# Kernel tuning notes

Measured on AMD Instinct MI355X. Metric: run time of the kernel, lower is better.

The kernel has to match this reference:

```python
import jax, jax.numpy as jnp
import numpy as np

TEMP = 0.2
LAM = 0.5
EPS = 1e-8

N, IN_SIZE, HID = 8192, 256, 128


def setup_inputs() -> dict:
    key = jax.random.key(0)
    k1, k2, k3, k4, k5 = jax.random.split(key, 5)
    z_mp = jax.random.normal(k1, (N, IN_SIZE), dtype=jnp.float32)
    z_sc = jax.random.normal(k2, (N, IN_SIZE), dtype=jnp.float32)
    # xavier-normal-ish init scale
    W1 = jax.random.normal(k3, (IN_SIZE, HID), dtype=jnp.float32) * (1.414 * (2.0 / (IN_SIZE + HID)) ** 0.5)
    b1 = jnp.zeros((HID,), dtype=jnp.float32)
    W2 = jax.random.normal(k4, (HID, HID), dtype=jnp.float32) * (1.414 * (2.0 / (HID + HID)) ** 0.5)
    b2 = jnp.zeros((HID,), dtype=jnp.float32)
    pos = jax.random.randint(k5, (N, N), 0, 2, dtype=jnp.int32)
    return {"z_mp": z_mp, "z_sc": z_sc, "W1": W1, "b1": b1, "W2": W2, "b2": b2, "pos": pos}


def _proj(z, W1, b1, W2, b2):
    # Linear -> ELU -> Linear
    return jax.nn.elu(z @ W1 + b1) @ W2 + b2


def _l2norm(z):
    # F.normalize(p=2, dim=1): torch uses clamp_min(eps) on the norm
    n = jnp.linalg.norm(z, axis=1, keepdims=True)
    return z / jnp.maximum(n, 1e-12)


def reference(z_mp, z_sc, W1, b1, W2, b2, pos):
    zp_sc = _proj(z_sc, W1, b1, W2, b2)
    zp_mp = _proj(z_mp, W1, b1, W2, b2)
    # exp(cosine similarity / temperature), dense N x N
    sim = jnp.exp(_l2norm(zp_mp) @ _l2norm(zp_sc).T / TEMP)  # [N, N] mp2sc
    mp2sc = sim / (jnp.sum(sim, axis=1, keepdims=True) + EPS)
    sc2mp = sim.T / (jnp.sum(sim, axis=0)[:, None] + EPS)
    posf = pos.astype(sim.dtype)
    lori_sc = -jnp.log(jnp.sum(sc2mp * posf, axis=-1) + EPS)
    lori_mp = -jnp.log(jnp.sum(mp2sc * posf, axis=-1) + EPS)
    ans = LAM * lori_mp + (1.0 - LAM) * lori_sc
    ans = jnp.where(jnp.isnan(ans) | jnp.isinf(ans), jnp.zeros((), ans.dtype), ans)
    return ans
```

## Files before the change

### kernel.cpp

```cpp
#include <hip/hip_runtime.h>
#include <math.h>

#define N_ROWS 8192
#define IN_SZ 256
#define HID 128
#define INV_TEMP 5.0f
#define EPSV 1e-8f

typedef short short8 __attribute__((ext_vector_type(8)));
typedef float f32x4 __attribute__((ext_vector_type(4)));

__device__ __forceinline__ ushort f2bf(float v) {
    unsigned b = __float_as_uint(v);
    return (ushort)((b + 0x7FFFu + ((b >> 16) & 1u)) >> 16);
}
__device__ __forceinline__ float bf2f(ushort u) {
    return __uint_as_float(((unsigned)u) << 16);
}

__device__ __forceinline__ void gl2lds16(const void* g, void* l) {
    __builtin_amdgcn_global_load_lds(
        (const __attribute__((address_space(1))) unsigned*)g,
        (__attribute__((address_space(3))) unsigned*)l, 16, 0, 0);
}

__global__ __launch_bounds__(256) void pack_kernel(
    const int* __restrict__ pos, unsigned* __restrict__ posbits,
    float* __restrict__ sums)
{
    const int t = threadIdx.x;
    if (blockIdx.x < 4) {
        float4 z4 = make_float4(0.f, 0.f, 0.f, 0.f);
        float* base = sums + (size_t)blockIdx.x * 8192 + t * 32;
#pragma unroll
        for (int i = 0; i < 8; ++i) *(float4*)(base + i * 4) = z4;
    }
    const size_t nthreads = (size_t)gridDim.x * 256;
    const size_t total_groups = (size_t)N_ROWS * N_ROWS / 4;
#pragma unroll 8
    for (size_t g = (size_t)blockIdx.x * 256 + t; g < total_groups; g += nthreads) {
        int4 v = *(const int4*)(pos + g * 4);
        unsigned nib = (v.x != 0 ? 1u : 0u) | (v.y != 0 ? 2u : 0u)
                     | (v.z != 0 ? 4u : 0u) | (v.w != 0 ? 8u : 0u);
        unsigned u = nib << ((t & 7) * 4);
        u |= (unsigned)__shfl_xor((int)u, 1);
        u |= (unsigned)__shfl_xor((int)u, 2);
        u |= (unsigned)__shfl_xor((int)u, 4);
        if ((t & 7) == 0) posbits[g >> 3] = u;
    }
}

__global__ __launch_bounds__(256) void proj_kernel(
    const float* __restrict__ z_mp, const float* __restrict__ z_sc,
    const float* __restrict__ W1, const float* __restrict__ b1,
    const float* __restrict__ W2, const float* __restrict__ b2,
    ushort* __restrict__ h_mp, ushort* __restrict__ l_mp,
    ushort* __restrict__ h_sc, ushort* __restrict__ l_sc)
{
    __shared__ float smem[10368];
    float* sZ  = smem;
    float* sW  = smem + 2176;
    float* sH  = smem;
    float* sW2 = smem + 4224;
    float* snorm = smem + 8320;

    const int t = threadIdx.x;
    const int sel = blockIdx.y;
    const int R0 = blockIdx.x * 32;
    const int tx = t & 15, ty = t >> 4;
    const float* z = (sel == 0) ? z_mp : z_sc;
    ushort* outH   = (sel == 0) ? h_mp : h_sc;
    ushort* outL   = (sel == 0) ? l_mp : l_sc;

    if (t < 32) snorm[t] = 0.f;

    float acc[2][8];
#pragma unroll
    for (int i = 0; i < 2; ++i)
#pragma unroll
        for (int j = 0; j < 8; ++j) acc[i][j] = 0.f;

    for (int ch = 0; ch < 4; ++ch) {
#pragma unroll
        for (int it = 0; it < 2; ++it) {
            int idx = it * 256 + t;
            int k4 = idx >> 5;
            int m  = idx & 31;
            float4 v = *(const float4*)(z + (size_t)(R0 + m) * IN_SZ + ch * 64 + k4 * 4);
            sZ[(k4 * 4 + 0) * 34 + m] = v.x;
            sZ[(k4 * 4 + 1) * 34 + m] = v.y;
            sZ[(k4 * 4 + 2) * 34 + m] = v.z;
            sZ[(k4 * 4 + 3) * 34 + m] = v.w;
        }
#pragma unroll
        for (int it = 0; it < 8; ++it) {
            int idx = it * 256 + t;
            int kk = idx >> 5;
            int c4 = idx & 31;
            *(float4*)(sW + kk * 128 + c4 * 4) =
                *(const float4*)(W1 + (size_t)(ch * 64 + kk) * HID + c4 * 4);
        }
        __syncthreads();
#pragma unroll 4
        for (int k = 0; k < 64; ++k) {
            float2 a = *(const float2*)(sZ + k * 34 + ty * 2);
            float4 b0 = *(float4*)(sW + k * 128 + tx * 4);
            float4 b1v = *(float4*)(sW + k * 128 + 64 + tx * 4);
            float av[2] = {a.x, a.y};
            float bv[8] = {b0.x, b0.y, b0.z, b0.w, b1v.x, b1v.y, b1v.z, b1v.w};
#pragma unroll
            for (int i = 0; i < 2; ++i)
#pragma unroll
                for (int j = 0; j < 8; ++j)
                    acc[i][j] = fmaf(av[i], bv[j], acc[i][j]);
        }
        __syncthreads();
    }

#pragma unroll
    for (int j = 0; j < 8; ++j) {
        int c = (j < 4) ? tx * 4 + j : 64 + tx * 4 + (j - 4);
        float bb = b1[c];
#pragma unroll
        for (int i = 0; i < 2; ++i) {
            float v = acc[i][j] + bb;
            v = (v > 0.f) ? v : (__expf(v) - 1.f);
            sH[c * 33 + ty * 2 + i] = v;
        }
    }

    float acc2[2][8];
#pragma unroll
    for (int i = 0; i < 2; ++i)
#pragma unroll
        for (int j = 0; j < 8; ++j) acc2[i][j] = 0.f;

    for (int ch2 = 0; ch2 < 4; ++ch2) {
#pragma unroll
        for (int it = 0; it < 4; ++it) {
            int idx = it * 256 + t;
            int kk = idx >> 5;
            int c4 = idx & 31;
            *(float4*)(sW2 + kk * 128 + c4 * 4) =
                *(const float4*)(W2 + (size_t)(ch2 * 32 + kk) * HID + c4 * 4);
        }
        __syncthreads();
#pragma unroll 4
        for (int k2 = 0; k2 < 32; ++k2) {
            float a0 = sH[(ch2 * 32 + k2) * 33 + ty * 2];
            float a1 = sH[(ch2 * 32 + k2) * 33 + ty * 2 + 1];
            float4 b0 = *(float4*)(sW2 + k2 * 128 + tx * 4);
            float4 b1v = *(float4*)(sW2 + k2 * 128 + 64 + tx * 4);
            float av[2] = {a0, a1};
            float bv[8] = {b0.x, b0.y, b0.z, b0.w, b1v.x, b1v.y, b1v.z, b1v.w};
#pragma unroll
            for (int i = 0; i < 2; ++i)
#pragma unroll
                for (int j = 0; j < 8; ++j)
                    acc2[i][j] = fmaf(av[i], bv[j], acc2[i][j]);
        }
        __syncthreads();
    }

#pragma unroll
    for (int j = 0; j < 8; ++j) {
        int c = (j < 4) ? tx * 4 + j : 64 + tx * 4 + (j - 4);
        float bb = b2[c];
#pragma unroll
        for (int i = 0; i < 2; ++i) acc2[i][j] += bb;
    }
#pragma unroll
    for (int i = 0; i < 2; ++i) {
        float p = 0.f;
#pragma unroll
        for (int j = 0; j < 8; ++j) p = fmaf(acc2[i][j], acc2[i][j], p);
        atomicAdd(&snorm[ty * 2 + i], p);
    }
    __syncthreads();
#pragma unroll
    for (int i = 0; i < 2; ++i) {
        int r = ty * 2 + i;
        float scale = 1.f / fmaxf(sqrtf(snorm[r]), 1e-12f);
#pragma unroll
        for (int half = 0; half < 2; ++half) {
            ushort4 h4, l4;
            ushort hu[4], lu[4];
#pragma unroll
            for (int j = 0; j < 4; ++j) {
                float v = acc2[i][half * 4 + j] * scale;
                ushort hb = f2bf(v);
                float lv = v - bf2f(hb);
                hu[j] = hb;
                lu[j] = f2bf(lv);
            }
            h4.x = hu[0]; h4.y = hu[1]; h4.z = hu[2]; h4.w = hu[3];
            l4.x = lu[0]; l4.y = lu[1]; l4.z = lu[2]; l4.w = lu[3];
            size_t off = (size_t)(R0 + r) * HID + half * 64 + tx * 4;
            *(ushort4*)(outH + off) = h4;
            *(ushort4*)(outL + off) = l4;
        }
    }
}

__global__ __launch_bounds__(256, 3) void sim_mfma_kernel(
    const ushort* __restrict__ mh_, const ushort* __restrict__ ml_,
    const ushort* __restrict__ sh_, const ushort* __restrict__ sl_,
    const unsigned* __restrict__ posbits, float* __restrict__ sums)
{
    __shared__ float redR[128], redRP[128], redC[128], redCP[128];
    __shared__ unsigned sBR[128][4];
    __shared__ unsigned sBC[128][4];
    __shared__ __align__(16) char stage[32768];

    const int t = threadIdx.x;
    const int lane = t & 63;
    const int wave = t >> 6;
    const int wr = wave >> 1, wc = wave & 1;
    const int I = blockIdx.y * 128;
    const int J = blockIdx.x * 128;
    const int r0 = wr * 64, c0 = wc * 64;
    const int lrow = lane & 15;
    const int quad = lane >> 4;

    uint4 pb;
    if (t < 128) pb = *(const uint4*)(posbits + (size_t)(I + t) * (N_ROWS / 32) + J / 32);
    else         pb = *(const uint4*)(posbits + (size_t)(J + t - 128) * (N_ROWS / 32) + I / 32);

    const char* mhB = (const char*)mh_;
    const char* mlB = (const char*)ml_;
    const char* shB = (const char*)sh_;
    const char* slB = (const char*)sl_;

    const int rsub = lane >> 2;
    const int cfetch = (lane & 3) ^ ((lane >> 3) & 3);
    const size_t ga0 = (size_t)(I + wave * 32 + rsub) * 256 + cfetch * 16;
    const size_t ga1 = ga0 + 16 * 256;
    const size_t gb0 = (size_t)(J + wave * 32 + rsub) * 256 + cfetch * 16;
    const size_t gb1 = gb0 + 16 * 256;
    char* sAh = stage;
    char* sAl = stage + 8192;
    char* sBh = stage + 16384;
    char* sBl = stage + 24576;
    const unsigned ls0 = wave * 2048, ls1 = ls0 + 1024;

    const int slot = quad ^ ((lrow >> 1) & 3);
    unsigned ra[4], rb[4];
#pragma unroll
    for (int s = 0; s < 4; ++s) {
        ra[s] = (unsigned)(r0 + s * 16 + lrow) * 64 + slot * 16;
        rb[s] = (unsigned)(c0 + s * 16 + lrow) * 64 + slot * 16;
    }

    f32x4 acc[4][4];
#pragma unroll
    for (int si = 0; si < 4; ++si)
#pragma unroll
        for (int sj = 0; sj < 4; ++sj) acc[si][sj] = (f32x4)0.f;

#pragma unroll
    for (int ks = 0; ks < 4; ++ks) {
        const unsigned kb = ks * 64;
        if (ks) __syncthreads();
        gl2lds16(mhB + ga0 + kb, sAh + ls0);
        gl2lds16(mhB + ga1 + kb, sAh + ls1);
        gl2lds16(mlB + ga0 + kb, sAl + ls0);
        gl2lds16(mlB + ga1 + kb, sAl + ls1);
        gl2lds16(shB + gb0 + kb, sBh + ls0);
        gl2lds16(shB + gb1 + kb, sBh + ls1);
        gl2lds16(slB + gb0 + kb, sBl + ls0);
        gl2lds16(slB + gb1 + kb, sBl + ls1);
        __syncthreads();

        short8 ah[4], bh[4];
#pragma unroll
        for (int s = 0; s < 4; ++s) ah[s] = *(const short8*)(sAh + ra[s]);
#pragma unroll
        for (int s = 0; s < 4; ++s) bh[s] = *(const short8*)(sBh + rb[s]);
#pragma unroll
        for (int si = 0; si < 4; ++si)
#pragma unroll
            for (int sj = 0; sj < 4; ++sj)
                acc[si][sj] = __builtin_amdgcn_mfma_f32_16x16x32_bf16(
                    ah[si], bh[sj], acc[si][sj], 0, 0, 0);

        short8 bl[4];
#pragma unroll
        for (int s = 0; s < 4; ++s) bl[s] = *(const short8*)(sBl + rb[s]);
#pragma unroll
        for (int si = 0; si < 4; ++si)
#pragma unroll
            for (int sj = 0; sj < 4; ++sj)
                acc[si][sj] = __builtin_amdgcn_mfma_f32_16x16x32_bf16(
                    ah[si], bl[sj], acc[si][sj], 0, 0, 0);

        short8 al[4];
#pragma unroll
        for (int s = 0; s < 4; ++s) al[s] = *(const short8*)(sAl + ra[s]);
#pragma unroll
        for (int si = 0; si < 4; ++si)
#pragma unroll
            for (int sj = 0; sj < 4; ++sj)
                acc[si][sj] = __builtin_amdgcn_mfma_f32_16x16x32_bf16(
                    al[si], bh[sj], acc[si][sj], 0, 0, 0);
    }

#pragma unroll
    for (int si = 0; si < 4; ++si)
#pragma unroll
        for (int sj = 0; sj < 4; ++sj)
#pragma unroll
            for (int r = 0; r < 4; ++r)
                acc[si][sj][r] = __expf(acc[si][sj][r] * INV_TEMP);

    if (t < 128) {
        redR[t] = 0.f; redRP[t] = 0.f;
        *(uint4*)sBR[t] = pb;
    } else {
        int u = t - 128;
        redC[u] = 0.f; redCP[u] = 0.f;
        *(uint4*)sBC[u] = pb;
    }
    __syncthreads();

#pragma unroll
    for (int sj = 0; sj < 4; ++sj) {
        int n = c0 + sj * 16 + lrow;
        float cs = 0.f, cp = 0.f;
#pragma unroll
        for (int si = 0; si < 4; ++si) {
            f32x4 v = acc[si][sj];
            cs += v[0] + v[1] + v[2] + v[3];
            int bb = r0 + si * 16 + quad * 4;
            unsigned bits = (sBC[n][bb >> 5] >> (bb & 31)) & 0xF;
            cp += (bits & 1u ? v[0] : 0.f) + (bits & 2u ? v[1] : 0.f)
                + (bits & 4u ? v[2] : 0.f) + (bits & 8u ? v[3] : 0.f);
        }
        cs += __shfl_xor(cs, 16); cs += __shfl_xor(cs, 32);
        cp += __shfl_xor(cp, 16); cp += __shfl_xor(cp, 32);
        if (lane < 16) {
            atomicAdd(&redC[c0 + sj * 16 + lane], cs);
            atomicAdd(&redCP[c0 + sj * 16 + lane], cp);
        }
    }

    float* tw = (float*)(stage + wave * 4352);
#pragma unroll
    for (int si = 0; si < 4; ++si) {
#pragma unroll
        for (int sj = 0; sj < 4; ++sj)
#pragma unroll
            for (int r = 0; r < 4; ++r)
                tw[(quad * 4 + r) * 68 + sj * 16 + lrow] = acc[si][sj][r];
        int row = lane & 15;
        int chunk = lane >> 4;
        const unsigned prw = sBR[r0 + si * 16 + row][(c0 >> 5) + (chunk >> 1)];
        float rs = 0.f, rp = 0.f;
#pragma unroll
        for (int c4 = 0; c4 < 4; ++c4) {
            f32x4 v = *(const f32x4*)(tw + row * 68 + chunk * 16 + c4 * 4);
            unsigned bits = (prw >> ((chunk & 1) * 16 + c4 * 4)) & 0xF;
            rs += v[0] + v[1] + v[2] + v[3];
            rp += (bits & 1u ? v[0] : 0.f) + (bits & 2u ? v[1] : 0.f)
                + (bits & 4u ? v[2] : 0.f) + (bits & 8u ? v[3] : 0.f);
        }
        rs += __shfl_xor(rs, 16); rs += __shfl_xor(rs, 32);
        rp += __shfl_xor(rp, 16); rp += __shfl_xor(rp, 32);
        if (lane < 16) {
            atomicAdd(&redR[r0 + si * 16 + lane], rs);
            atomicAdd(&redRP[r0 + si * 16 + lane], rp);
        }
    }
    __syncthreads();

    if (t < 128) {
        atomicAdd(&sums[I + t],              redR[t]);
        atomicAdd(&sums[N_ROWS + I + t],     redRP[t]);
        atomicAdd(&sums[2 * N_ROWS + J + t], redC[t]);
        atomicAdd(&sums[3 * N_ROWS + J + t], redCP[t]);
    }
}

__global__ __launch_bounds__(256) void finish_kernel(
    const float* __restrict__ sums, float* __restrict__ out)
{
    int i = blockIdx.x * 256 + threadIdx.x;
    if (i >= N_ROWS) return;
    float rsv = sums[i];
    float rpv = sums[N_ROWS + i];
    float csv = sums[2 * N_ROWS + i];
    float cpv = sums[3 * N_ROWS + i];
    float lmp = -logf(rpv / (rsv + EPSV) + EPSV);
    float lsc = -logf(cpv / (csv + EPSV) + EPSV);
    float a = 0.5f * lmp + 0.5f * lsc;
    if (!isfinite(a)) a = 0.f;
    out[i] = a;
}

extern "C" void kernel_launch(void* const* d_in, const int* in_sizes, int n_in,
                              void* d_out, int out_size, void* d_ws, size_t ws_size,
                              hipStream_t stream) {
    const float* z_mp = (const float*)d_in[0];
    const float* z_sc = (const float*)d_in[1];
    const float* W1   = (const float*)d_in[2];
    const float* b1   = (const float*)d_in[3];
    const float* W2   = (const float*)d_in[4];
    const float* b2   = (const float*)d_in[5];
    const int*   pos  = (const int*)d_in[6];
    float* out = (float*)d_out;

    ushort* wsu = (ushort*)d_ws;
    const size_t NV = (size_t)N_ROWS * HID;
    ushort* mh = wsu;
    ushort* ml = wsu + NV;
    ushort* sh = wsu + 2 * NV;
    ushort* sl = wsu + 3 * NV;
    float* sums = (float*)(wsu + 4 * NV);
    unsigned* posbits = (unsigned*)(sums + 4 * N_ROWS);

    pack_kernel<<<2048, 256, 0, stream>>>(pos, posbits, sums);
    proj_kernel<<<dim3(256, 2), 256, 0, stream>>>(
        z_mp, z_sc, W1, b1, W2, b2, mh, ml, sh, sl);
    sim_mfma_kernel<<<dim3(64, 64), 256, 0, stream>>>(mh, ml, sh, sl, posbits, sums);
    finish_kernel<<<N_ROWS / 256, 256, 0, stream>>>(sums, out);
}
```

Before: 482.6 us.

## Replace split-bf16 three-pass similarity GEMM with single fp16 MFMA pass

The normalized projections were stored as bf16 high/low pairs, and the similarity GEMM ran three MFMA passes to emulate near-fp32 precision. They are now stored as a single fp16 value, and the GEMM runs one fp16 MFMA pass. This cuts MFMA work to a third and halves the operand loads into shared memory. The LDS staging is reorganized into 128-byte rows with an XOR swizzle and two K steps. Because the inputs are unit-normalized, fp16 keeps more mantissa bits than bf16, but the lost low part may affect accuracy after exp(x/0.2).

```diff
diff --git a/kernel.cpp b/kernel.cpp
--- a/kernel.cpp
+++ b/kernel.cpp
@@ -7,15 +7,13 @@
 #define INV_TEMP 5.0f
 #define EPSV 1e-8f
 
-typedef short short8 __attribute__((ext_vector_type(8)));
+typedef _Float16 half8 __attribute__((ext_vector_type(8)));
 typedef float f32x4 __attribute__((ext_vector_type(4)));
 
-__device__ __forceinline__ ushort f2bf(float v) {
-    unsigned b = __float_as_uint(v);
-    return (ushort)((b + 0x7FFFu + ((b >> 16) & 1u)) >> 16);
-}
-__device__ __forceinline__ float bf2f(ushort u) {
-    return __uint_as_float(((unsigned)u) << 16);
+__device__ __forceinline__ ushort f2h(float v) {
+    union { _Float16 h; ushort u; } c;
+    c.h = (_Float16)v;
+    return c.u;
 }
 
 __device__ __forceinline__ void gl2lds16(const void* g, void* l) {
@@ -54,8 +52,7 @@
     const float* __restrict__ z_mp, const float* __restrict__ z_sc,
     const float* __restrict__ W1, const float* __restrict__ b1,
     const float* __restrict__ W2, const float* __restrict__ b2,
-    ushort* __restrict__ h_mp, ushort* __restrict__ l_mp,
-    ushort* __restrict__ h_sc, ushort* __restrict__ l_sc)
+    ushort* __restrict__ h_mp, ushort* __restrict__ h_sc)
 {
     __shared__ float smem[10368];
     float* sZ  = smem;
@@ -70,7 +67,6 @@
     const int tx = t & 15, ty = t >> 4;
     const float* z = (sel == 0) ? z_mp : z_sc;
     ushort* outH   = (sel == 0) ? h_mp : h_sc;
-    ushort* outL   = (sel == 0) ? l_mp : l_sc;
 
     if (t < 32) snorm[t] = 0.f;
 
@@ -183,28 +179,19 @@
         float scale = 1.f / fmaxf(sqrtf(snorm[r]), 1e-12f);
 #pragma unroll
         for (int half = 0; half < 2; ++half) {
-            ushort4 h4, l4;
-            ushort hu[4], lu[4];
-#pragma unroll
-            for (int j = 0; j < 4; ++j) {
-                float v = acc2[i][half * 4 + j] * scale;
-                ushort hb = f2bf(v);
-                float lv = v - bf2f(hb);
-                hu[j] = hb;
-                lu[j] = f2bf(lv);
-            }
-            h4.x = hu[0]; h4.y = hu[1]; h4.z = hu[2]; h4.w = hu[3];
-            l4.x = lu[0]; l4.y = lu[1]; l4.z = lu[2]; l4.w = lu[3];
+            ushort4 h4;
+            h4.x = f2h(acc2[i][half * 4 + 0] * scale);
+            h4.y = f2h(acc2[i][half * 4 + 1] * scale);
+            h4.z = f2h(acc2[i][half * 4 + 2] * scale);
+            h4.w = f2h(acc2[i][half * 4 + 3] * scale);
             size_t off = (size_t)(R0 + r) * HID + half * 64 + tx * 4;
             *(ushort4*)(outH + off) = h4;
-            *(ushort4*)(outL + off) = l4;
         }
     }
 }
 
 __global__ __launch_bounds__(256, 3) void sim_mfma_kernel(
-    const ushort* __restrict__ mh_, const ushort* __restrict__ ml_,
-    const ushort* __restrict__ sh_, const ushort* __restrict__ sl_,
+    const ushort* __restrict__ mh_, const ushort* __restrict__ sh_,
     const unsigned* __restrict__ posbits, float* __restrict__ sums)
 {
     __shared__ float redR[128], redRP[128], redC[128], redCP[128];
@@ -227,29 +214,23 @@
     else         pb = *(const uint4*)(posbits + (size_t)(J + t - 128) * (N_ROWS / 32) + I / 32);
 
     const char* mhB = (const char*)mh_;
-    const char* mlB = (const char*)ml_;
     const char* shB = (const char*)sh_;
-    const char* slB = (const char*)sl_;
-
-    const int rsub = lane >> 2;
-    const int cfetch = (lane & 3) ^ ((lane >> 3) & 3);
-    const size_t ga0 = (size_t)(I + wave * 32 + rsub) * 256 + cfetch * 16;
-    const size_t ga1 = ga0 + 16 * 256;
-    const size_t gb0 = (size_t)(J + wave * 32 + rsub) * 256 + cfetch * 16;
-    const size_t gb1 = gb0 + 16 * 256;
-    char* sAh = stage;
-    char* sAl = stage + 8192;
-    char* sBh = stage + 16384;
-    char* sBl = stage + 24576;
-    const unsigned ls0 = wave * 2048, ls1 = ls0 + 1024;
-
-    const int slot = quad ^ ((lrow >> 1) & 3);
+
+    const int rsub = lane >> 3;
+    const int cfetch = (lane & 7) ^ rsub;
+    const size_t gaBase = (size_t)(I + wave * 32 + rsub) * 256 + cfetch * 16;
+    const size_t gbBase = (size_t)(J + wave * 32 + rsub) * 256 + cfetch * 16;
+    char* sA = stage;
+    char* sB = stage + 16384;
+    const unsigned lsw = wave * 4096;
+
     unsigned ra[4], rb[4];
 #pragma unroll
     for (int s = 0; s < 4; ++s) {
-        ra[s] = (unsigned)(r0 + s * 16 + lrow) * 64 + slot * 16;
-        rb[s] = (unsigned)(c0 + s * 16 + lrow) * 64 + slot * 16;
-    }
+        ra[s] = (unsigned)(r0 + s * 16 + lrow) * 128;
+        rb[s] = (unsigned)(c0 + s * 16 + lrow) * 128;
+    }
+    const unsigned sl7 = (unsigned)(lrow & 7);
 
     f32x4 acc[4][4];
 #pragma unroll
@@ -258,50 +239,30 @@
         for (int sj = 0; sj < 4; ++sj) acc[si][sj] = (f32x4)0.f;
 
 #pragma unroll
-    for (int ks = 0; ks < 4; ++ks) {
-        const unsigned kb = ks * 64;
+    for (int ks = 0; ks < 2; ++ks) {
         if (ks) __syncthreads();
-        gl2lds16(mhB + ga0 + kb, sAh + ls0);
-        gl2lds16(mhB + ga1 + kb, sAh + ls1);
-        gl2lds16(mlB + ga0 + kb, sAl + ls0);
-        gl2lds16(mlB + ga1 + kb, sAl + ls1);
-        gl2lds16(shB + gb0 + kb, sBh + ls0);
-        gl2lds16(shB + gb1 + kb, sBh + ls1);
-        gl2lds16(slB + gb0 + kb, sBl + ls0);
-        gl2lds16(slB + gb1 + kb, sBl + ls1);
-        __syncthreads();
-
-        short8 ah[4], bh[4];
-#pragma unroll
-        for (int s = 0; s < 4; ++s) ah[s] = *(const short8*)(sAh + ra[s]);
-#pragma unroll
-        for (int s = 0; s < 4; ++s) bh[s] = *(const short8*)(sBh + rb[s]);
-#pragma unroll
-        for (int si = 0; si < 4; ++si)
-#pragma unroll
-            for (int sj = 0; sj < 4; ++sj)
-                acc[si][sj] = __builtin_amdgcn_mfma_f32_16x16x32_bf16(
-                    ah[si], bh[sj], acc[si][sj], 0, 0, 0);
-
-        short8 bl[4];
-#pragma unroll
-        for (int s = 0; s < 4; ++s) bl[s] = *(const short8*)(sBl + rb[s]);
-#pragma unroll
-        for (int si = 0; si < 4; ++si)
-#pragma unroll
-            for (int sj = 0; sj < 4; ++sj)
-                acc[si][sj] = __builtin_amdgcn_mfma_f32_16x16x32_bf16(
-                    ah[si], bl[sj], acc[si][sj], 0, 0, 0);
-
-        short8 al[4];
-#pragma unroll
-        for (int s = 0; s < 4; ++s) al[s] = *(const short8*)(sAl + ra[s]);
-#pragma unroll
-        for (int si = 0; si < 4; ++si)
-#pragma unroll
-            for (int sj = 0; sj < 4; ++sj)
-                acc[si][sj] = __builtin_amdgcn_mfma_f32_16x16x32_bf16(
-                    al[si], bh[sj], acc[si][sj], 0, 0, 0);
+#pragma unroll
+        for (int i = 0; i < 4; ++i) {
+            gl2lds16(mhB + gaBase + i * 2048 + ks * 128, sA + lsw + i * 1024);
+            gl2lds16(shB + gbBase + i * 2048 + ks * 128, sB + lsw + i * 1024);
+        }
+        __syncthreads();
+
+#pragma unroll
+        for (int h = 0; h < 2; ++h) {
+            const unsigned slot = ((unsigned)(quad + h * 4) ^ sl7) * 16;
+            half8 a[4], b[4];
+#pragma unroll
+            for (int s = 0; s < 4; ++s) a[s] = *(const half8*)(sA + ra[s] + slot);
+#pragma unroll
+            for (int s = 0; s < 4; ++s) b[s] = *(const half8*)(sB + rb[s] + slot);
+#pragma unroll
+            for (int si = 0; si < 4; ++si)
+#pragma unroll
+                for (int sj = 0; sj < 4; ++sj)
+                    acc[si][sj] = __builtin_amdgcn_mfma_f32_16x16x32_f16(
+                        a[si], b[sj], acc[si][sj], 0, 0, 0);
+        }
     }
 
 #pragma unroll
@@ -411,15 +372,13 @@
     ushort* wsu = (ushort*)d_ws;
     const size_t NV = (size_t)N_ROWS * HID;
     ushort* mh = wsu;
-    ushort* ml = wsu + NV;
-    ushort* sh = wsu + 2 * NV;
-    ushort* sl = wsu + 3 * NV;
-    float* sums = (float*)(wsu + 4 * NV);
+    ushort* sh = wsu + NV;
+    float* sums = (float*)(wsu + 2 * NV);
     unsigned* posbits = (unsigned*)(sums + 4 * N_ROWS);
 
     pack_kernel<<<2048, 256, 0, stream>>>(pos, posbits, sums);
     proj_kernel<<<dim3(256, 2), 256, 0, stream>>>(
-        z_mp, z_sc, W1, b1, W2, b2, mh, ml, sh, sl);
-    sim_mfma_kernel<<<dim3(64, 64), 256, 0, stream>>>(mh, ml, sh, sl, posbits, sums);
+        z_mp, z_sc, W1, b1, W2, b2, mh, sh);
+    sim_mfma_kernel<<<dim3(64, 64), 256, 0, stream>>>(mh, sh, posbits, sums);
     finish_kernel<<<N_ROWS / 256, 256, 0, stream>>>(sums, out);
 }
```

Measured after the change: 457.9 us. 5.1% less time.
